# Performance work log

Hardware: AMD Instinct MI355X
Metric: run time of the kernel (lower is better)

Reference implementation:

```python
import jax, jax.numpy as jnp
import numpy as np

B, C_IN, C_OUT, RED, H, W = 8, 256, 64, 16, 256, 256
K = 3


def setup_inputs() -> dict:
    key = jax.random.key(0)
    k1, k2, k3, k4, k5 = jax.random.split(key, 5)
    x = jax.random.normal(k1, (B, C_OUT, H, W), dtype=jnp.float32)
    vec = jax.random.normal(k2, (B, C_IN), dtype=jnp.float32)
    # ChanNorm affine params
    g = jnp.ones((1, C_OUT, 1, 1), dtype=jnp.float32)
    b = jnp.zeros((1, C_OUT, 1, 1), dtype=jnp.float32)
    # conv_du MLP (torch Linear weights: [out, in], no bias)
    w1 = jax.random.normal(k3, (C_IN // RED, C_IN), dtype=jnp.float32) / np.sqrt(C_IN)
    w2 = jax.random.normal(k4, (C_OUT, C_IN // RED), dtype=jnp.float32) / np.sqrt(C_IN // RED)
    # Conv2DMod weight, kaiming normal fan_in (leaky_relu a=0): std=sqrt(2/fan_in)
    fan_in = C_OUT * K * K
    wconv = jax.random.normal(k5, (C_OUT, C_OUT, K, K), dtype=jnp.float32) * np.sqrt(2.0 / fan_in)
    return {"x": x, "vec": vec, "g": g, "b": b, "w1": w1, "w2": w2, "wconv": wconv}


def reference(x, vec, g, b, w1, w2, wconv):
    eps_norm = 1e-5
    eps_mod = 1e-8
    # ChanNorm: normalize over channel dim (unbiased=False var)
    mean = jnp.mean(x, axis=1, keepdims=True)
    var = jnp.mean((x - mean) ** 2, axis=1, keepdims=True)
    nx = (x - mean) / jnp.sqrt(var + eps_norm) * g + b
    # style MLP: Linear -> LeakyReLU(0.1) -> Linear (no biases)
    hid = jax.nn.leaky_relu(vec @ w1.T, negative_slope=0.1)
    sty = hid @ w2.T  # [B, C_OUT]
    # per-sample modulated weights: [B, O, I, K, K]
    weights = wconv[None, :, :, :, :] * (sty[:, None, :, None, None] + 1.0)
    # demodulate
    d = jax.lax.rsqrt(jnp.sum(weights ** 2, axis=(2, 3, 4), keepdims=True) + eps_mod)
    weights = weights * d
    # grouped conv with groups=B == per-sample conv; same padding for k=3,s=1,d=1 -> 1
    pad = ((H - 1) * 0 + 1 * (K - 1)) // 2
    def per_sample_conv(xi, wi):
        # xi: [C,H,W], wi: [O,I,K,K]
        return jax.lax.conv_general_dilated(
            xi[None], wi, window_strides=(1, 1),
            padding=[(pad, pad), (pad, pad)],
            dimension_numbers=("NCHW", "OIHW", "NCHW"))[0]
    out = jax.vmap(per_sample_conv)(nx, weights)  # [B, O, H, W]
    return out + x
```

## Files before the change

kernel.cpp:

```cpp
#include <hip/hip_runtime.h>
#include <hip/hip_bf16.h>

typedef __hip_bfloat16 bf16;
typedef __attribute__((ext_vector_type(8))) short short8;
typedef __attribute__((ext_vector_type(4))) float float4v;

#define Hd 256
#define Wd 256
#define HW 65536
#define CO 64

__global__ __launch_bounds__(64) void k1_style(
    const float* __restrict__ vec, const float* __restrict__ w1,
    const float* __restrict__ w2, const float* __restrict__ wconv,
    bf16* __restrict__ wA)
{
    int o = blockIdx.x;
    int s = blockIdx.y;
    int i = threadIdx.x;

    float sv[4];
#pragma unroll
    for (int q = 0; q < 4; ++q) sv[q] = vec[s * 256 + q * 64 + i];

    float hid[16];
#pragma unroll
    for (int j = 0; j < 16; ++j) {
        float p = 0.f;
#pragma unroll
        for (int q = 0; q < 4; ++q) p += sv[q] * w1[j * 256 + q * 64 + i];
#pragma unroll
        for (int off = 32; off >= 1; off >>= 1) p += __shfl_xor(p, off, 64);
        hid[j] = p > 0.f ? p : 0.1f * p;
    }
    float sty = 0.f;
#pragma unroll
    for (int j = 0; j < 16; ++j) sty += w2[i * 16 + j] * hid[j];
    float msty = sty + 1.0f;

    float wrow[9];
#pragma unroll
    for (int tt = 0; tt < 9; ++tt) wrow[tt] = wconv[(o * 64 + i) * 9 + tt] * msty;
    float ss = 0.f;
#pragma unroll
    for (int tt = 0; tt < 9; ++tt) ss += wrow[tt] * wrow[tt];
#pragma unroll
    for (int off = 32; off >= 1; off >>= 1) ss += __shfl_xor(ss, off, 64);
    float d = rsqrtf(ss + 1e-8f);

    bf16* wAs = wA + s * (18 * 64 * 32);
#pragma unroll
    for (int tt = 0; tt < 9; ++tt) {
        int k = tt * 64 + i;
        wAs[(k >> 5) * 2048 + o * 32 + (k & 31)] = (bf16)(wrow[tt] * d);
    }
}

__global__ __launch_bounds__(256) void k2_norm(
    const float* __restrict__ x, const float* __restrict__ gg,
    const float* __restrict__ bb, bf16* __restrict__ nxT)
{
    __shared__ float sg[64], sb[64];
    int t = threadIdx.x;
    if (t < 64) { sg[t] = gg[t]; sb[t] = bb[t]; }
    __syncthreads();

    int s  = blockIdx.y;
    int px = blockIdx.x * 256 + t;
    int h  = px >> 8, w = px & 255;

    const float* xs = x + (size_t)s * (CO * HW) + px;
    float v[64];
    float s1 = 0.f, s2 = 0.f;
#pragma unroll
    for (int c = 0; c < 64; ++c) {
        float f = xs[(size_t)c * HW];
        v[c] = f; s1 += f; s2 += f * f;
    }
    float mean = s1 * (1.f / 64);
    float var  = s2 * (1.f / 64) - mean * mean;
    float rstd = rsqrtf(var + 1e-5f);

    bf16* dst = nxT + ((size_t)(s * Hd + h) * 8 * Wd + w) * 8;
#pragma unroll
    for (int c8 = 0; c8 < 8; ++c8) {
        bf16 ov[8];
#pragma unroll
        for (int k = 0; k < 8; ++k) {
            int c = c8 * 8 + k;
            ov[k] = (bf16)((v[c] - mean) * rstd * sg[c] + sb[c]);
        }
        *(uint4*)&dst[(size_t)c8 * (Wd * 8)] = *(uint4*)ov;
    }
}

#define SLOT_ELEMS (8 * 68 * 8)
__global__ __launch_bounds__(256, 4) void k3_conv(
    const bf16* __restrict__ nxT, const bf16* __restrict__ wA,
    const float* __restrict__ x, float* __restrict__ out)
{
    int w0 = blockIdx.x * 64;
    int h0 = blockIdx.y * 8;
    int s  = blockIdx.z;
    int t  = threadIdx.x;
    __shared__ __align__(16) bf16 tile[4 * SLOT_ELEMS];

    int wave = t >> 6;
    int lane = t & 63;
    int col  = lane & 15;
    int quad = lane >> 4;

    const bf16* wAs = wA + s * (18 * 64 * 32);
    short8 afrag[18];
#pragma unroll
    for (int kc = 0; kc < 18; ++kc) {
        union { uint4 u; short8 s8; } a;
        a.u = *(const uint4*)&wAs[kc * 2048 + (wave * 16 + col) * 32 + quad * 8];
        afrag[kc] = a.s8;
    }

    auto stage_row_now = [&](int g) {
        bf16* dst = tile + ((g + 4) & 3) * SLOT_ELEMS;
        const bf16* src = nxT + (size_t)(s * Hd + g) * (8 * Wd * 8);
        bool gok = (g >= 0 && g < Hd);
#pragma unroll
        for (int j = 0; j < 3; ++j) {
            int idx = j * 256 + t;
            if (idx < 528) {
                int c8 = idx / 66;
                int wl = idx - c8 * 66;
                int wabs = w0 + wl - 1;
                uint4 v = make_uint4(0u, 0u, 0u, 0u);
                if (gok && wabs >= 0 && wabs < Wd)
                    v = *(const uint4*)&src[(c8 * Wd + wabs) * 8];
                *(uint4*)&dst[(c8 * 68 + wl) * 8] = v;
            }
        }
    };

    stage_row_now(h0 - 1);
    stage_row_now(h0);
    stage_row_now(h0 + 1);
    __syncthreads();

#pragma unroll 1
    for (int r = 0; r < 8; ++r) {
        int grow = h0 + r;

        uint4 stg[3];
        int   soff[3];
        bool  sdo[3];
        int g2 = grow + 2;
        bool do_stage = (r < 7);
        bool gok = do_stage && (g2 >= 0 && g2 < Hd);
        const bf16* src = nxT + (size_t)(s * Hd + g2) * (8 * Wd * 8);
#pragma unroll
        for (int j = 0; j < 3; ++j) {
            int idx = j * 256 + t;
            sdo[j] = do_stage && (idx < 528);
            int c8 = idx / 66;
            int wl = idx - c8 * 66;
            int wabs = w0 + wl - 1;
            soff[j] = (c8 * 68 + wl) * 8;
            stg[j] = make_uint4(0u, 0u, 0u, 0u);
            if (sdo[j] && gok && wabs >= 0 && wabs < Wd)
                stg[j] = *(const uint4*)&src[(c8 * Wd + wabs) * 8];
        }

        float4v acc[4];
#pragma unroll
        for (int nt = 0; nt < 4; ++nt) acc[nt] = (float4v)0.f;

#pragma unroll
        for (int kc = 0; kc < 18; ++kc) {
            int tap = kc >> 1;
            int kh = tap / 3, kw = tap - kh * 3;
            int ch8 = (kc & 1) * 4 + quad;
            const bf16* slotp = tile + ((grow - 1 + kh + 4) & 3) * SLOT_ELEMS;
#pragma unroll
            for (int nt = 0; nt < 4; ++nt) {
                int wl = nt * 16 + col + kw;
                union { uint4 u; short8 s8; } b;
                b.u = *(const uint4*)&slotp[(ch8 * 68 + wl) * 8];
                acc[nt] = __builtin_amdgcn_mfma_f32_16x16x32_bf16(
                    afrag[kc], b.s8, acc[nt], 0, 0, 0);
            }
        }

        bf16* sdst = tile + ((g2 + 4) & 3) * SLOT_ELEMS;
#pragma unroll
        for (int j = 0; j < 3; ++j)
            if (sdo[j]) *(uint4*)&sdst[soff[j]] = stg[j];

#pragma unroll
        for (int nt = 0; nt < 4; ++nt) {
#pragma unroll
            for (int rr = 0; rr < 4; ++rr) {
                int o = wave * 16 + quad * 4 + rr;
                int w = w0 + nt * 16 + col;
                size_t idx = (size_t)(s * CO + o) * HW + grow * Wd + w;
                out[idx] = acc[nt][rr] + x[idx];
            }
        }
        __syncthreads();
    }
}

extern "C" void kernel_launch(void* const* d_in, const int* in_sizes, int n_in,
                              void* d_out, int out_size, void* d_ws, size_t ws_size,
                              hipStream_t stream)
{
    const float* x     = (const float*)d_in[0];
    const float* vec   = (const float*)d_in[1];
    const float* g     = (const float*)d_in[2];
    const float* bb    = (const float*)d_in[3];
    const float* w1    = (const float*)d_in[4];
    const float* w2    = (const float*)d_in[5];
    const float* wconv = (const float*)d_in[6];
    float* out = (float*)d_out;

    bf16* wA  = (bf16*)d_ws;
    bf16* nxT = (bf16*)((char*)d_ws + (1u << 20));

    k1_style<<<dim3(64, 8), 64, 0, stream>>>(vec, w1, w2, wconv, wA);
    k2_norm<<<dim3(256, 8), 256, 0, stream>>>(x, g, bb, nxT);
    k3_conv<<<dim3(4, 32, 8), 256, 0, stream>>>(nxT, wA, x, out);
}
```

Measured before the change: 382.3 us.

## Fuse channel norm into conv kernel, recomputing halo tiles in shared memory

Removes the separate normalization kernel and its bf16 intermediate buffer. Each conv block now reads x directly, computes per-pixel channel mean/variance for a 10x34 halo tile, and writes normalized bf16 values into shared memory. The conv then runs over 8 rows from that tile with a 2x2 wave split over output channels and pixel columns, and no per-row restaging or barriers. The trade-off is recomputing normalization on halo pixels (about 1.3x extra reads of x) and a serial prologue with no overlap between loading and MFMA work. Tiles are also narrower (32 pixels).

New measurement: 315.0 us. -17.6%, faster.

```diff
diff --git a/kernel.cpp b/kernel.cpp
--- a/kernel.cpp
+++ b/kernel.cpp
@@ -56,153 +56,100 @@
     }
 }
 
-__global__ __launch_bounds__(256) void k2_norm(
+#define PXB 32
+#define ROWS 8
+#define TR 10
+#define WL 34
+#define ROW_ELEMS (8 * WL * 8)
+
+__global__ __launch_bounds__(256, 2) void k3_fused(
     const float* __restrict__ x, const float* __restrict__ gg,
-    const float* __restrict__ bb, bf16* __restrict__ nxT)
+    const float* __restrict__ bb, const bf16* __restrict__ wA,
+    float* __restrict__ out)
 {
+    int w0 = blockIdx.x * PXB;
+    int h0 = blockIdx.y * ROWS;
+    int s  = blockIdx.z;
+    int t  = threadIdx.x;
+    __shared__ __align__(16) bf16 tile[TR * ROW_ELEMS];
     __shared__ float sg[64], sb[64];
-    int t = threadIdx.x;
     if (t < 64) { sg[t] = gg[t]; sb[t] = bb[t]; }
     __syncthreads();
 
-    int s  = blockIdx.y;
-    int px = blockIdx.x * 256 + t;
-    int h  = px >> 8, w = px & 255;
+    for (int p = t; p < TR * WL; p += 256) {
+        int dr = p / WL, wl = p - dr * WL;
+        int grow = h0 + dr - 1, wabs = w0 + wl - 1;
+        bf16* dst = &tile[dr * ROW_ELEMS + wl * 8];
+        if (grow >= 0 && grow < Hd && wabs >= 0 && wabs < Wd) {
+            const float* xp = x + (size_t)s * (CO * HW) + (size_t)grow * Wd + wabs;
+            float v[64], s1 = 0.f, s2 = 0.f;
+#pragma unroll
+            for (int c = 0; c < 64; ++c) {
+                float f = xp[(size_t)c * HW];
+                v[c] = f; s1 += f; s2 += f * f;
+            }
+            float mean = s1 * (1.f / 64);
+            float var  = s2 * (1.f / 64) - mean * mean;
+            float rstd = rsqrtf(var + 1e-5f);
+#pragma unroll
+            for (int c8 = 0; c8 < 8; ++c8) {
+                bf16 ov[8];
+#pragma unroll
+                for (int k = 0; k < 8; ++k) {
+                    int c = c8 * 8 + k;
+                    ov[k] = (bf16)((v[c] - mean) * rstd * sg[c] + sb[c]);
+                }
+                *(uint4*)&dst[c8 * (WL * 8)] = *(uint4*)ov;
+            }
+        } else {
+            uint4 z = make_uint4(0u, 0u, 0u, 0u);
+#pragma unroll
+            for (int c8 = 0; c8 < 8; ++c8) *(uint4*)&dst[c8 * (WL * 8)] = z;
+        }
+    }
+    __syncthreads();
 
-    const float* xs = x + (size_t)s * (CO * HW) + px;
-    float v[64];
-    float s1 = 0.f, s2 = 0.f;
-#pragma unroll
-    for (int c = 0; c < 64; ++c) {
-        float f = xs[(size_t)c * HW];
-        v[c] = f; s1 += f; s2 += f * f;
-    }
-    float mean = s1 * (1.f / 64);
-    float var  = s2 * (1.f / 64) - mean * mean;
-    float rstd = rsqrtf(var + 1e-5f);
-
-    bf16* dst = nxT + ((size_t)(s * Hd + h) * 8 * Wd + w) * 8;
-#pragma unroll
-    for (int c8 = 0; c8 < 8; ++c8) {
-        bf16 ov[8];
-#pragma unroll
-        for (int k = 0; k < 8; ++k) {
-            int c = c8 * 8 + k;
-            ov[k] = (bf16)((v[c] - mean) * rstd * sg[c] + sb[c]);
-        }
-        *(uint4*)&dst[(size_t)c8 * (Wd * 8)] = *(uint4*)ov;
-    }
-}
-
-#define SLOT_ELEMS (8 * 68 * 8)
-__global__ __launch_bounds__(256, 4) void k3_conv(
-    const bf16* __restrict__ nxT, const bf16* __restrict__ wA,
-    const float* __restrict__ x, float* __restrict__ out)
-{
-    int w0 = blockIdx.x * 64;
-    int h0 = blockIdx.y * 8;
-    int s  = blockIdx.z;
-    int t  = threadIdx.x;
-    __shared__ __align__(16) bf16 tile[4 * SLOT_ELEMS];
-
-    int wave = t >> 6;
-    int lane = t & 63;
-    int col  = lane & 15;
-    int quad = lane >> 4;
+    int wave = t >> 6, lane = t & 63;
+    int mi = wave & 1, ni = wave >> 1;
+    int col = lane & 15, quad = lane >> 4;
 
     const bf16* wAs = wA + s * (18 * 64 * 32);
-    short8 afrag[18];
+    short8 afrag[18][2];
 #pragma unroll
-    for (int kc = 0; kc < 18; ++kc) {
-        union { uint4 u; short8 s8; } a;
-        a.u = *(const uint4*)&wAs[kc * 2048 + (wave * 16 + col) * 32 + quad * 8];
-        afrag[kc] = a.s8;
-    }
-
-    auto stage_row_now = [&](int g) {
-        bf16* dst = tile + ((g + 4) & 3) * SLOT_ELEMS;
-        const bf16* src = nxT + (size_t)(s * Hd + g) * (8 * Wd * 8);
-        bool gok = (g >= 0 && g < Hd);
+    for (int kc = 0; kc < 18; ++kc)
 #pragma unroll
-        for (int j = 0; j < 3; ++j) {
-            int idx = j * 256 + t;
-            if (idx < 528) {
-                int c8 = idx / 66;
-                int wl = idx - c8 * 66;
-                int wabs = w0 + wl - 1;
-                uint4 v = make_uint4(0u, 0u, 0u, 0u);
-                if (gok && wabs >= 0 && wabs < Wd)
-                    v = *(const uint4*)&src[(c8 * Wd + wabs) * 8];
-                *(uint4*)&dst[(c8 * 68 + wl) * 8] = v;
-            }
-        }
-    };
-
-    stage_row_now(h0 - 1);
-    stage_row_now(h0);
-    stage_row_now(h0 + 1);
-    __syncthreads();
-
-#pragma unroll 1
-    for (int r = 0; r < 8; ++r) {
-        int grow = h0 + r;
-
-        uint4 stg[3];
-        int   soff[3];
-        bool  sdo[3];
-        int g2 = grow + 2;
-        bool do_stage = (r < 7);
-        bool gok = do_stage && (g2 >= 0 && g2 < Hd);
-        const bf16* src = nxT + (size_t)(s * Hd + g2) * (8 * Wd * 8);
-#pragma unroll
-        for (int j = 0; j < 3; ++j) {
-            int idx = j * 256 + t;
-            sdo[j] = do_stage && (idx < 528);
-            int c8 = idx / 66;
-            int wl = idx - c8 * 66;
-            int wabs = w0 + wl - 1;
-            soff[j] = (c8 * 68 + wl) * 8;
-            stg[j] = make_uint4(0u, 0u, 0u, 0u);
-            if (sdo[j] && gok && wabs >= 0 && wabs < Wd)
-                stg[j] = *(const uint4*)&src[(c8 * Wd + wabs) * 8];
+        for (int mt = 0; mt < 2; ++mt) {
+            union { uint4 u; short8 s8; } a;
+            a.u = *(const uint4*)&wAs[kc * 2048 + (mi * 32 + mt * 16 + col) * 32 + quad * 8];
+            afrag[kc][mt] = a.s8;
         }
 
-        float4v acc[4];
-#pragma unroll
-        for (int nt = 0; nt < 4; ++nt) acc[nt] = (float4v)0.f;
-
+#pragma unroll 2
+    for (int r = 0; r < ROWS; ++r) {
+        float4v acc[2];
+        acc[0] = (float4v)0.f; acc[1] = (float4v)0.f;
 #pragma unroll
         for (int kc = 0; kc < 18; ++kc) {
             int tap = kc >> 1;
             int kh = tap / 3, kw = tap - kh * 3;
             int ch8 = (kc & 1) * 4 + quad;
-            const bf16* slotp = tile + ((grow - 1 + kh + 4) & 3) * SLOT_ELEMS;
+            int wl = ni * 16 + col + kw;
+            union { uint4 u; short8 s8; } b;
+            b.u = *(const uint4*)&tile[(r + kh) * ROW_ELEMS + (ch8 * WL + wl) * 8];
+            acc[0] = __builtin_amdgcn_mfma_f32_16x16x32_bf16(afrag[kc][0], b.s8, acc[0], 0, 0, 0);
+            acc[1] = __builtin_amdgcn_mfma_f32_16x16x32_bf16(afrag[kc][1], b.s8, acc[1], 0, 0, 0);
+        }
+        int grow = h0 + r;
+        int wpx  = w0 + ni * 16 + col;
 #pragma unroll
-            for (int nt = 0; nt < 4; ++nt) {
-                int wl = nt * 16 + col + kw;
-                union { uint4 u; short8 s8; } b;
-                b.u = *(const uint4*)&slotp[(ch8 * 68 + wl) * 8];
-                acc[nt] = __builtin_amdgcn_mfma_f32_16x16x32_bf16(
-                    afrag[kc], b.s8, acc[nt], 0, 0, 0);
+        for (int mt = 0; mt < 2; ++mt) {
+#pragma unroll
+            for (int rr = 0; rr < 4; ++rr) {
+                int o = mi * 32 + mt * 16 + quad * 4 + rr;
+                size_t idx = (size_t)(s * CO + o) * HW + (size_t)grow * Wd + wpx;
+                out[idx] = acc[mt][rr] + x[idx];
             }
         }
-
-        bf16* sdst = tile + ((g2 + 4) & 3) * SLOT_ELEMS;
-#pragma unroll
-        for (int j = 0; j < 3; ++j)
-            if (sdo[j]) *(uint4*)&sdst[soff[j]] = stg[j];
-
-#pragma unroll
-        for (int nt = 0; nt < 4; ++nt) {
-#pragma unroll
-            for (int rr = 0; rr < 4; ++rr) {
-                int o = wave * 16 + quad * 4 + rr;
-                int w = w0 + nt * 16 + col;
-                size_t idx = (size_t)(s * CO + o) * HW + grow * Wd + w;
-                out[idx] = acc[nt][rr] + x[idx];
-            }
-        }
-        __syncthreads();
     }
 }
 
@@ -219,10 +166,8 @@
     const float* wconv = (const float*)d_in[6];
     float* out = (float*)d_out;
 
-    bf16* wA  = (bf16*)d_ws;
-    bf16* nxT = (bf16*)((char*)d_ws + (1u << 20));
+    bf16* wA = (bf16*)d_ws;
 
     k1_style<<<dim3(64, 8), 64, 0, stream>>>(vec, w1, w2, wconv, wA);
-    k2_norm<<<dim3(256, 8), 256, 0, stream>>>(x, g, bb, nxT);
-    k3_conv<<<dim3(4, 32, 8), 256, 0, stream>>>(nxT, wA, x, out);
+    k3_fused<<<dim3(8, 32, 8), 256, 0, stream>>>(x, g, bb, wA, out);
 }
```
